# Performance work log

Measured on AMD Instinct MI355X. Metric: run time of the kernel, lower is better.

## Reference

```python
import jax, jax.numpy as jnp
import numpy as np

T, A, E, N, W, HID, FD = 4096, 1024, 512, 32768, 10, 150, 20
GI = 2 * A + E  # 2560
BINS = jnp.array([1, 2, 3, 4, 8, 16, 32, 64], dtype=jnp.int32)


def _mlp(x, W1, b1, W2, b2, W3, b3):
    # Score module: Linear->ReLU->Linear->ReLU->Linear->1 (dropout is a no-op in eval)
    h = jax.nn.relu(x @ W1 + b1)
    h = jax.nn.relu(h @ W2 + b2)
    return h @ W3 + b3


def setup_inputs() -> dict:
    key = jax.random.key(0)
    ks = jax.random.split(key, 20)
    s = 0.02
    inp = {
        "states": jax.random.normal(ks[0], (T, A), jnp.float32),
        "embeds": jax.random.normal(ks[1], (T, E), jnp.float32),
        "span_starts": jax.random.randint(ks[2], (N,), 0, T - W, jnp.int32),
        "span_widths": jax.random.randint(ks[3], (N,), 1, W + 1, jnp.int32),
        # attention Score params (input A)
        "Wa1": jax.random.normal(ks[4], (A, HID)) * s, "ba1": jnp.zeros((HID,)),
        "Wa2": jax.random.normal(ks[5], (HID, HID)) * s, "ba2": jnp.zeros((HID,)),
        "Wa3": jax.random.normal(ks[6], (HID, 1)) * s, "ba3": jnp.zeros((1,)),
        # width Feature embedding table: len(bins)+1 = 9 rows
        "width_emb": jax.random.normal(ks[7], (9, FD)) * s,
        # mention Score params (input GI + FD)
        "Ws1": jax.random.normal(ks[8], (GI + FD, HID)) * s, "bs1": jnp.zeros((HID,)),
        "Ws2": jax.random.normal(ks[9], (HID, HID)) * s, "bs2": jnp.zeros((HID,)),
        "Ws3": jax.random.normal(ks[10], (HID, 1)) * s, "bs3": jnp.zeros((1,)),
    }
    return inp


def reference(states, embeds, span_starts, span_widths,
              Wa1, ba1, Wa2, ba2, Wa3, ba3, width_emb,
              Ws1, bs1, Ws2, bs2, Ws3, bs3):
    # per-token attention logits  [T]
    attns = _mlp(states, Wa1, ba1, Wa2, ba2, Wa3, ba3).squeeze(-1)
    offs = jnp.arange(W)                                   # [W]
    pos = span_starts[:, None] + offs[None, :]             # [N, W]
    mask = offs[None, :] < span_widths[:, None]            # ragged span mask
    pos_c = jnp.clip(pos, 0, T - 1)
    logit = jnp.where(mask, attns[pos_c], -jnp.inf)        # [N, W]
    w = jax.nn.softmax(logit, axis=1)                      # per-span softmax
    attn_sum = jnp.einsum('nw,nwe->ne', w, embeds[pos_c])  # [N, E]
    ends = span_starts + span_widths - 1
    bin_idx = jnp.sum(span_widths[:, None] >= BINS[None, :], axis=1)
    size = width_emb[bin_idx]                              # [N, FD]
    g = jnp.concatenate([states[span_starts], states[ends], attn_sum, size], axis=1)
    scores = _mlp(g, Ws1, bs1, Ws2, bs2, Ws3, bs3).squeeze(-1)  # [N]
    return scores
```

## Files before the change

kernel.cpp:

```cpp
#include <hip/hip_runtime.h>
#include <math.h>

#define T_TOK 4096
#define A_DIM 1024
#define E_DIM 512
#define N_SPAN 32768
#define W_MAX 10
#define HID 150
#define FD 20

#define PR  160
#define KP2 160

#define WS_ATTNS 0
#define WS_PB    4096
#define WS_WPACK 1314816
#define WS_SB    1627856
#define WS_EB    3725008
#define PB_P0 0
#define PB_P1 655360
#define PB_P2 1310720
#define PB_P3 1966080
#define WP_ST  0
#define WP_V   491520
#define WP_A2  573440
#define WP_S2  599040
#define WP_WE1 624640
#define WP_TOTAL 626080
#define SB_PIECES 524288
#define EB_PIECES 262144
#define PK_ITEMS (WP_TOTAL + SB_PIECES + EB_PIECES)

typedef short  bf16x8 __attribute__((ext_vector_type(8)));
typedef float  f32x4  __attribute__((ext_vector_type(4)));

__device__ __forceinline__ float4 ld4(const float* p) { return *(const float4*)p; }

__device__ __forceinline__ unsigned short f2bf(float f) {
    unsigned u = __float_as_uint(f);
    unsigned r = u + 0x7fffu + ((u >> 16) & 1u);
    return (unsigned short)(r >> 16);
}
__device__ __forceinline__ float bf2f(short s) {
    return __uint_as_float(((unsigned)(unsigned short)s) << 16);
}
__device__ __forceinline__ bf16x8 cvt_frag(const float* p) {
    float4 u = ld4(p), v = ld4(p + 4);
    bf16x8 f;
    f[0] = (short)f2bf(u.x); f[1] = (short)f2bf(u.y);
    f[2] = (short)f2bf(u.z); f[3] = (short)f2bf(u.w);
    f[4] = (short)f2bf(v.x); f[5] = (short)f2bf(v.y);
    f[6] = (short)f2bf(v.z); f[7] = (short)f2bf(v.w);
    return f;
}

typedef const __attribute__((address_space(1))) unsigned int as1_u32;
typedef __attribute__((address_space(3))) unsigned int as3_u32;
__device__ __forceinline__ void dma16(const void* g, void* l) {
    __builtin_amdgcn_global_load_lds((as1_u32*)g, (as3_u32*)l, 16, 0, 0);
}
template<int N> __device__ __forceinline__ void waitv() {
    asm volatile("s_waitcnt vmcnt(%0)" :: "n"(N) : "memory");
}

__global__ __launch_bounds__(256) void prepack_kernel(
    const float* __restrict__ states, const float* __restrict__ embeds,
    const float* __restrict__ Wa1, const float* __restrict__ Ws1,
    const float* __restrict__ Wa2, const float* __restrict__ Ws2,
    const float* __restrict__ width_emb,
    unsigned short* __restrict__ wp, unsigned short* __restrict__ Sb,
    unsigned short* __restrict__ Eb)
{
    int idx = blockIdx.x * 256 + threadIdx.x;
    if (idx >= PK_ITEMS) return;
    if (idx < WP_TOTAL) {
        float v = 0.f;
        if (idx < WP_V) {
            int gidx = idx / 163840, r = idx % 163840;
            int ngrp = r / 81920, r2 = r % 81920;
            int c = r2 / 2560, d = r2 % 2560;
            int n = d >> 5, qsw = (d >> 3) & 3, off = d & 7;
            int q = qsw ^ ((n >> 1) & 3);
            int k = c * 32 + q * 8 + off;
            int gn = ngrp * 80 + n;
            const float* W = (gidx == 0) ? Wa1 : Ws1 + (size_t)(gidx - 1) * 1024 * HID;
            if (gn < HID) v = W[(size_t)k * HID + gn];
        } else if (idx < WP_A2) {
            int r = idx - WP_V;
            int ngrp = r / 40960, r2 = r % 40960;
            int c = r2 / 2560, d = r2 % 2560;
            int n = d >> 5, qsw = (d >> 3) & 3, off = d & 7;
            int q = qsw ^ ((n >> 1) & 3);
            int k = c * 32 + q * 8 + off;
            int gn = ngrp * 80 + n;
            if (gn < HID) v = Ws1[(size_t)(2048 + k) * HID + gn];
        } else if (idx < WP_S2) {
            int e = idx - WP_A2;
            int n = e / KP2, k = e % KP2;
            if (n < HID && k < HID) v = Wa2[(size_t)k * HID + n];
        } else if (idx < WP_WE1) {
            int e = idx - WP_S2;
            int n = e / KP2, k = e % KP2;
            if (n < HID && k < HID) v = Ws2[(size_t)k * HID + n];
        } else {
            int e = idx - WP_WE1;
            int b = e / KP2, n = e % KP2;
            if (n < HID)
                for (int k = 0; k < FD; ++k)
                    v = fmaf(width_emb[b * FD + k], Ws1[(size_t)(2560 + k) * HID + n], v);
        }
        wp[idx] = f2bf(v);
    } else if (idx < WP_TOTAL + SB_PIECES) {
        int p = idx - WP_TOTAL;
        int mb = p >> 11, r = p & 2047;
        int c = r >> 6, d8 = r & 63;
        int m = d8 >> 2, qsw = d8 & 3;
        int q = qsw ^ ((m >> 1) & 3);
        const float* src = states + (size_t)(mb * 16 + m) * A_DIM + c * 32 + q * 8;
        *(bf16x8*)(Sb + (size_t)p * 8) = cvt_frag(src);
    } else {
        int p = idx - WP_TOTAL - SB_PIECES;
        int mb = p >> 10, r = p & 1023;
        int c = r >> 6, d8 = r & 63;
        int m = d8 >> 2, qsw = d8 & 3;
        int q = qsw ^ ((m >> 1) & 3);
        const float* src = embeds + (size_t)(mb * 16 + m) * E_DIM + c * 32 + q * 8;
        *(bf16x8*)(Eb + (size_t)p * 8) = cvt_frag(src);
    }
}

template<int NC>
__device__ __forceinline__ void gemm_dma(
    const unsigned short* __restrict__ srcA, const unsigned short* __restrict__ srcB,
    unsigned short (*__restrict__ bufB)[2560], unsigned short (*__restrict__ bufA)[512],
    int lane, int l15, int quad, f32x4 (&acc)[5])
{
    const int swz = (quad ^ ((l15 >> 1) & 3)) * 8;
    const int bl = l15 * 32 + swz;
#define DMAC(c) { _Pragma("unroll")                                          \
        for (int i = 0; i < 5; ++i)                                          \
            dma16(srcB + (size_t)(c) * 2560 + i * 512 + lane * 8,            \
                  &bufB[(c) % 3][i * 512]);                                  \
        dma16(srcA + (size_t)(c) * 512 + lane * 8, &bufA[(c) % 3][0]); }
    DMAC(0);
    DMAC(1);
#pragma unroll
    for (int c = 0; c < NC; ++c) {
        if (c + 2 < NC) DMAC(c + 2);
        if (c + 2 < NC)      waitv<12>();
        else if (c + 1 < NC) waitv<6>();
        else                 waitv<0>();
        bf16x8 af = *(const bf16x8*)(&bufA[c % 3][0] + bl);
        const unsigned short* bb = &bufB[c % 3][0];
#pragma unroll
        for (int t = 0; t < 5; ++t) {
            bf16x8 bf = *(const bf16x8*)(bb + t * 512 + bl);
            acc[t] = __builtin_amdgcn_mfma_f32_16x16x32_bf16(af, bf, acc[t], 0, 0, 0);
        }
    }
#undef DMAC
}

__global__ __launch_bounds__(128) void token_kernel(
    const unsigned short* __restrict__ Sb, const unsigned short* __restrict__ Eb,
    const unsigned short* __restrict__ wp, unsigned short* __restrict__ Pb,
    const float* __restrict__ ba1, const float* __restrict__ ba2,
    const float* __restrict__ Wa3, const float* __restrict__ ba3,
    float* __restrict__ attns)
{
    __shared__ __align__(16) unsigned short bufB[2][3][2560];
    __shared__ __align__(16) unsigned short bufA[2][3][512];
    __shared__ float sPartA[2][16];

    const int wv = threadIdx.x >> 6;
    const int lane = threadIdx.x & 63, l15 = lane & 15, quad = lane >> 4;
    const int task = blockIdx.x;
    const int ngrp = wv;

    f32x4 acc[5];
#pragma unroll
    for (int t = 0; t < 5; ++t)
#pragma unroll
        for (int i = 0; i < 4; ++i) acc[t][i] = 0.f;

    int m0, gidx;
    if (task < 768) {
        const int mb = task / 3;
        m0 = mb * 16;
        gidx = task % 3;
        const unsigned short* srcA = Sb + (size_t)mb * 16384;
        const unsigned short* srcB = wp + WP_ST + gidx * 163840 + ngrp * 81920;
        gemm_dma<32>(srcA, srcB, bufB[wv], bufA[wv], lane, l15, quad, acc);
    } else {
        const int mb = task - 768;
        m0 = mb * 16;
        gidx = 3;
        const unsigned short* srcA = Eb + (size_t)mb * 8192;
        const unsigned short* srcB = wp + WP_V + ngrp * 40960;
        gemm_dma<16>(srcA, srcB, bufB[wv], bufA[wv], lane, l15, quad, acc);
    }

    if (gidx == 0) {
        unsigned short (*sHb)[168] = (unsigned short (*)[168])&bufB[0][0][0];
        __syncthreads();
#pragma unroll
        for (int t = 0; t < 5; ++t) {
            const int col = ngrp * 80 + t * 16 + l15;
            const float b1 = (col < HID) ? ba1[col] : 0.f;
#pragma unroll
            for (int i = 0; i < 4; ++i)
                sHb[quad * 4 + i][col] = f2bf(fmaxf(acc[t][i] + b1, 0.f));
        }
        __syncthreads();
        f32x4 a2[5];
#pragma unroll
        for (int t = 0; t < 5; ++t)
#pragma unroll
            for (int i = 0; i < 4; ++i) a2[t][i] = 0.f;
#pragma unroll
        for (int c = 0; c < 5; ++c) {
            const int kq = c * 32 + quad * 8;
            bf16x8 af = *(const bf16x8*)&sHb[l15][kq];
#pragma unroll
            for (int t = 0; t < 5; ++t) {
                const int nt = ngrp * 5 + t;
                bf16x8 bf = *(const bf16x8*)(wp + WP_A2 +
                            (size_t)(nt * 16 + l15) * KP2 + kq);
                a2[t] = __builtin_amdgcn_mfma_f32_16x16x32_bf16(af, bf, a2[t], 0, 0, 0);
            }
        }
        float sc[4] = {0.f, 0.f, 0.f, 0.f};
#pragma unroll
        for (int t = 0; t < 5; ++t) {
            const int col = (ngrp * 5 + t) * 16 + l15;
            const float w3 = (col < HID) ? Wa3[col] : 0.f;
            const float b2 = (col < HID) ? ba2[col] : 0.f;
#pragma unroll
            for (int i = 0; i < 4; ++i)
                sc[i] = fmaf(fmaxf(a2[t][i] + b2, 0.f), w3, sc[i]);
        }
#pragma unroll
        for (int off = 8; off >= 1; off >>= 1)
#pragma unroll
            for (int i = 0; i < 4; ++i) sc[i] += __shfl_down(sc[i], off, 16);
        if (l15 == 0)
#pragma unroll
            for (int i = 0; i < 4; ++i) sPartA[ngrp][quad * 4 + i] = sc[i];
        __syncthreads();
        if (threadIdx.x < 16)
            attns[m0 + threadIdx.x] =
                sPartA[0][threadIdx.x] + sPartA[1][threadIdx.x] + ba3[0];
    } else {
        unsigned short* Pg = Pb + (size_t)gidx * 655360;
#pragma unroll
        for (int t = 0; t < 5; ++t) {
            const int col = ngrp * 80 + t * 16 + l15;
#pragma unroll
            for (int i = 0; i < 4; ++i)
                Pg[(size_t)(m0 + quad * 4 + i) * PR + col] =
                    (col < HID) ? f2bf(acc[t][i]) : (unsigned short)0;
        }
    }
}

__global__ __launch_bounds__(256) void span_kernel(
    const unsigned short* __restrict__ Pb, const float* __restrict__ attns,
    const unsigned short* __restrict__ wp,
    const int* __restrict__ span_starts, const int* __restrict__ span_widths,
    const float* __restrict__ bs1, const float* __restrict__ bs2,
    const float* __restrict__ Ws3, const float* __restrict__ bs3,
    float* __restrict__ out)
{
    __shared__ unsigned short sHb[32][168];
    __shared__ float s_wgt[32][W_MAX];
    __shared__ int s_st[32], s_wd[32], s_bin[32], s_oid[32], s_wdr[32];
    __shared__ float sPart[4][32];
    __shared__ float sb1[KP2];

    const int tid = threadIdx.x;
    const int n0s = blockIdx.x * 32;

    if (tid < KP2) sb1[tid] = (tid < HID) ? bs1[tid] : 0.f;
    int st = 0, wd = 0;
    if (tid < 32) {
        st = span_starts[n0s + tid];
        wd = span_widths[n0s + tid];
        s_wdr[tid] = wd;
    }
    __syncthreads();
    if (tid < 32) {
        int rank = 0;
#pragma unroll
        for (int j = 0; j < 32; ++j) {
            const int wj = s_wdr[j];
            rank += (wj < wd) || (wj == wd && j < tid);
        }
        s_st[rank] = st; s_wd[rank] = wd; s_oid[rank] = tid;
        s_bin[rank] = (wd >= 1) + (wd >= 2) + (wd >= 3) + (wd >= 4) +
                      (wd >= 8) + (wd >= 16) + (wd >= 32) + (wd >= 64);
        float lg[W_MAX];
        float m = -1e30f;
#pragma unroll
        for (int w = 0; w < W_MAX; ++w)
            if (w < wd) { float a = attns[st + w]; lg[w] = a; m = fmaxf(m, a); }
        float sum = 0.f;
#pragma unroll
        for (int w = 0; w < W_MAX; ++w) {
            float e = (w < wd) ? __expf(lg[w] - m) : 0.f;
            lg[w] = e; sum += e;
        }
        float inv = 1.f / sum;
#pragma unroll
        for (int w = 0; w < W_MAX; ++w) s_wgt[rank][w] = lg[w] * inv;
    }
    __syncthreads();

    {
        const unsigned short* P1b = Pb + PB_P1;
        const unsigned short* P2b = Pb + PB_P2;
        const unsigned short* P3b = Pb + PB_P3;
        const unsigned short* WEb = wp + WP_WE1;
        const int s = tid >> 3, jl = tid & 7;
        const int sst = s_st[s], swd = s_wd[s];
        const size_t rs = (size_t)sst * PR;
        const size_t re = (size_t)(sst + swd - 1) * PR;
        const size_t rb = (size_t)s_bin[s] * PR;
        for (int c = jl; c < 20; c += 8) {
            const int j = c * 8;
            bf16x8 u1 = *(const bf16x8*)(P1b + rs + j);
            bf16x8 u2 = *(const bf16x8*)(P2b + re + j);
            bf16x8 uw = *(const bf16x8*)(WEb + rb + j);
            float acc[8];
#pragma unroll
            for (int i = 0; i < 8; ++i)
                acc[i] = bf2f(u1[i]) + bf2f(u2[i]) + bf2f(uw[i]) + sb1[j + i];
#pragma unroll
            for (int w = 0; w < W_MAX; ++w) {
                if (w < swd) {
                    float wt = s_wgt[s][w];
                    bf16x8 uv = *(const bf16x8*)(P3b + rs + (size_t)w * PR + j);
#pragma unroll
                    for (int i = 0; i < 8; ++i)
                        acc[i] = fmaf(wt, bf2f(uv[i]), acc[i]);
                }
            }
            bf16x8 pk;
#pragma unroll
            for (int i = 0; i < 8; ++i) pk[i] = (short)f2bf(fmaxf(acc[i], 0.f));
            *(bf16x8*)&sHb[s][j] = pk;
        }
    }
    __syncthreads();

    const int wv = tid >> 6, lane = tid & 63, l15 = lane & 15, quad = lane >> 4;
    const int nb = (wv < 2) ? wv * 3 : 6 + (wv - 2) * 2;
    const int cnt = (wv < 2) ? 3 : 2;

    f32x4 a2[2][3];
#pragma unroll
    for (int mt = 0; mt < 2; ++mt)
#pragma unroll
        for (int t = 0; t < 3; ++t)
#pragma unroll
            for (int i = 0; i < 4; ++i) a2[mt][t][i] = 0.f;

#pragma unroll
    for (int c = 0; c < 5; ++c) {
        int k0 = c * 32;
        bf16x8 af0 = *(const bf16x8*)&sHb[l15][k0 + quad * 8];
        bf16x8 af1 = *(const bf16x8*)&sHb[16 + l15][k0 + quad * 8];
#pragma unroll
        for (int t = 0; t < 3; ++t) {
            if (t < cnt) {
                bf16x8 b = *(const bf16x8*)(wp + WP_S2 +
                            (size_t)((nb + t) * 16 + l15) * KP2 + k0 + quad * 8);
                a2[0][t] = __builtin_amdgcn_mfma_f32_16x16x32_bf16(af0, b, a2[0][t], 0, 0, 0);
                a2[1][t] = __builtin_amdgcn_mfma_f32_16x16x32_bf16(af1, b, a2[1][t], 0, 0, 0);
            }
        }
    }

    float sc[2][4];
#pragma unroll
    for (int mt = 0; mt < 2; ++mt)
#pragma unroll
        for (int i = 0; i < 4; ++i) sc[mt][i] = 0.f;
#pragma unroll
    for (int t = 0; t < 3; ++t) {
        if (t < cnt) {
            int col = (nb + t) * 16 + l15;
            float w3 = (col < HID) ? Ws3[col] : 0.f;
            float b2 = (col < HID) ? bs2[col] : 0.f;
#pragma unroll
            for (int mt = 0; mt < 2; ++mt)
#pragma unroll
                for (int i = 0; i < 4; ++i)
                    sc[mt][i] = fmaf(fmaxf(a2[mt][t][i] + b2, 0.f), w3, sc[mt][i]);
        }
    }
#pragma unroll
    for (int off = 8; off >= 1; off >>= 1)
#pragma unroll
        for (int mt = 0; mt < 2; ++mt)
#pragma unroll
            for (int i = 0; i < 4; ++i)
                sc[mt][i] += __shfl_down(sc[mt][i], off, 16);
    if (l15 == 0) {
#pragma unroll
        for (int mt = 0; mt < 2; ++mt)
#pragma unroll
            for (int i = 0; i < 4; ++i)
                sPart[wv][mt * 16 + quad * 4 + i] = sc[mt][i];
    }
    __syncthreads();
    if (tid < 32)
        out[n0s + s_oid[tid]] = sPart[0][tid] + sPart[1][tid] + sPart[2][tid] +
                                sPart[3][tid] + bs3[0];
}

extern "C" void kernel_launch(void* const* d_in, const int* in_sizes, int n_in,
                              void* d_out, int out_size, void* d_ws, size_t ws_size,
                              hipStream_t stream)
{
    const float* states      = (const float*)d_in[0];
    const float* embeds      = (const float*)d_in[1];
    const int*   span_starts = (const int*)d_in[2];
    const int*   span_widths = (const int*)d_in[3];
    const float* Wa1 = (const float*)d_in[4];
    const float* ba1 = (const float*)d_in[5];
    const float* Wa2 = (const float*)d_in[6];
    const float* ba2 = (const float*)d_in[7];
    const float* Wa3 = (const float*)d_in[8];
    const float* ba3 = (const float*)d_in[9];
    const float* width_emb = (const float*)d_in[10];
    const float* Ws1 = (const float*)d_in[11];
    const float* bs1 = (const float*)d_in[12];
    const float* Ws2 = (const float*)d_in[13];
    const float* bs2 = (const float*)d_in[14];
    const float* Ws3 = (const float*)d_in[15];
    const float* bs3 = (const float*)d_in[16];
    float* out = (float*)d_out;

    float* ws    = (float*)d_ws;
    float* attns = ws + WS_ATTNS;
    unsigned short* Pb    = (unsigned short*)(ws + WS_PB);
    unsigned short* wpack = (unsigned short*)(ws + WS_WPACK);
    unsigned short* Sb    = (unsigned short*)(ws + WS_SB);
    unsigned short* Eb    = (unsigned short*)(ws + WS_EB);

    hipLaunchKernelGGL(prepack_kernel, dim3((PK_ITEMS + 255) / 256), dim3(256), 0, stream,
                       states, embeds, Wa1, Ws1, Wa2, Ws2, width_emb,
                       wpack, Sb, Eb);
    hipLaunchKernelGGL(token_kernel, dim3(1024), dim3(128), 0, stream,
                       Sb, Eb, wpack, Pb, ba1, ba2, Wa3, ba3, attns);
    hipLaunchKernelGGL(span_kernel, dim3(N_SPAN / 32), dim3(256), 0, stream,
                       Pb, attns, wpack, span_starts, span_widths,
                       bs1, bs2, Ws3, bs3, out);
}
```

Baseline: 139.9 us.

## Fuse fp32-to-bf16 activation conversion into token GEMM A-operand loads

Removes the prepack pass that converted states and embeds to swizzled bf16 buffers. The token GEMM now loads fp32 activations straight from global memory into registers, two float4 per chunk with a three-deep register prefetch, and converts them to bf16 before the MFMA. This drops a full read and write of the activations plus the A-side LDS staging. In exchange, each of the three column-group tasks that share a row block re-reads the fp32 rows, so global A traffic per task doubles, and register pressure rises.

```diff
diff --git a/kernel.cpp b/kernel.cpp
--- a/kernel.cpp
+++ b/kernel.cpp
@@ -15,8 +15,6 @@
 #define WS_ATTNS 0
 #define WS_PB    4096
 #define WS_WPACK 1314816
-#define WS_SB    1627856
-#define WS_EB    3725008
 #define PB_P0 0
 #define PB_P1 655360
 #define PB_P2 1310720
@@ -27,9 +25,6 @@
 #define WP_S2  599040
 #define WP_WE1 624640
 #define WP_TOTAL 626080
-#define SB_PIECES 524288
-#define EB_PIECES 262144
-#define PK_ITEMS (WP_TOTAL + SB_PIECES + EB_PIECES)
 
 typedef short  bf16x8 __attribute__((ext_vector_type(8)));
 typedef float  f32x4  __attribute__((ext_vector_type(4)));
@@ -44,15 +39,6 @@
 __device__ __forceinline__ float bf2f(short s) {
     return __uint_as_float(((unsigned)(unsigned short)s) << 16);
 }
-__device__ __forceinline__ bf16x8 cvt_frag(const float* p) {
-    float4 u = ld4(p), v = ld4(p + 4);
-    bf16x8 f;
-    f[0] = (short)f2bf(u.x); f[1] = (short)f2bf(u.y);
-    f[2] = (short)f2bf(u.z); f[3] = (short)f2bf(u.w);
-    f[4] = (short)f2bf(v.x); f[5] = (short)f2bf(v.y);
-    f[6] = (short)f2bf(v.z); f[7] = (short)f2bf(v.w);
-    return f;
-}
 
 typedef const __attribute__((address_space(1))) unsigned int as1_u32;
 typedef __attribute__((address_space(3))) unsigned int as3_u32;
@@ -64,93 +50,81 @@
 }
 
 __global__ __launch_bounds__(256) void prepack_kernel(
-    const float* __restrict__ states, const float* __restrict__ embeds,
     const float* __restrict__ Wa1, const float* __restrict__ Ws1,
     const float* __restrict__ Wa2, const float* __restrict__ Ws2,
     const float* __restrict__ width_emb,
-    unsigned short* __restrict__ wp, unsigned short* __restrict__ Sb,
-    unsigned short* __restrict__ Eb)
+    unsigned short* __restrict__ wp)
 {
     int idx = blockIdx.x * 256 + threadIdx.x;
-    if (idx >= PK_ITEMS) return;
-    if (idx < WP_TOTAL) {
-        float v = 0.f;
-        if (idx < WP_V) {
-            int gidx = idx / 163840, r = idx % 163840;
-            int ngrp = r / 81920, r2 = r % 81920;
-            int c = r2 / 2560, d = r2 % 2560;
-            int n = d >> 5, qsw = (d >> 3) & 3, off = d & 7;
-            int q = qsw ^ ((n >> 1) & 3);
-            int k = c * 32 + q * 8 + off;
-            int gn = ngrp * 80 + n;
-            const float* W = (gidx == 0) ? Wa1 : Ws1 + (size_t)(gidx - 1) * 1024 * HID;
-            if (gn < HID) v = W[(size_t)k * HID + gn];
-        } else if (idx < WP_A2) {
-            int r = idx - WP_V;
-            int ngrp = r / 40960, r2 = r % 40960;
-            int c = r2 / 2560, d = r2 % 2560;
-            int n = d >> 5, qsw = (d >> 3) & 3, off = d & 7;
-            int q = qsw ^ ((n >> 1) & 3);
-            int k = c * 32 + q * 8 + off;
-            int gn = ngrp * 80 + n;
-            if (gn < HID) v = Ws1[(size_t)(2048 + k) * HID + gn];
-        } else if (idx < WP_S2) {
-            int e = idx - WP_A2;
-            int n = e / KP2, k = e % KP2;
-            if (n < HID && k < HID) v = Wa2[(size_t)k * HID + n];
-        } else if (idx < WP_WE1) {
-            int e = idx - WP_S2;
-            int n = e / KP2, k = e % KP2;
-            if (n < HID && k < HID) v = Ws2[(size_t)k * HID + n];
-        } else {
-            int e = idx - WP_WE1;
-            int b = e / KP2, n = e % KP2;
-            if (n < HID)
-                for (int k = 0; k < FD; ++k)
-                    v = fmaf(width_emb[b * FD + k], Ws1[(size_t)(2560 + k) * HID + n], v);
-        }
-        wp[idx] = f2bf(v);
-    } else if (idx < WP_TOTAL + SB_PIECES) {
-        int p = idx - WP_TOTAL;
-        int mb = p >> 11, r = p & 2047;
-        int c = r >> 6, d8 = r & 63;
-        int m = d8 >> 2, qsw = d8 & 3;
-        int q = qsw ^ ((m >> 1) & 3);
-        const float* src = states + (size_t)(mb * 16 + m) * A_DIM + c * 32 + q * 8;
-        *(bf16x8*)(Sb + (size_t)p * 8) = cvt_frag(src);
+    if (idx >= WP_TOTAL) return;
+    float v = 0.f;
+    if (idx < WP_V) {
+        int gidx = idx / 163840, r = idx % 163840;
+        int ngrp = r / 81920, r2 = r % 81920;
+        int c = r2 / 2560, d = r2 % 2560;
+        int n = d >> 5, qsw = (d >> 3) & 3, off = d & 7;
+        int q = qsw ^ ((n >> 1) & 3);
+        int k = c * 32 + q * 8 + off;
+        int gn = ngrp * 80 + n;
+        const float* W = (gidx == 0) ? Wa1 : Ws1 + (size_t)(gidx - 1) * 1024 * HID;
+        if (gn < HID) v = W[(size_t)k * HID + gn];
+    } else if (idx < WP_A2) {
+        int r = idx - WP_V;
+        int ngrp = r / 40960, r2 = r % 40960;
+        int c = r2 / 2560, d = r2 % 2560;
+        int n = d >> 5, qsw = (d >> 3) & 3, off = d & 7;
+        int q = qsw ^ ((n >> 1) & 3);
+        int k = c * 32 + q * 8 + off;
+        int gn = ngrp * 80 + n;
+        if (gn < HID) v = Ws1[(size_t)(2048 + k) * HID + gn];
+    } else if (idx < WP_S2) {
+        int e = idx - WP_A2;
+        int n = e / KP2, k = e % KP2;
+        if (n < HID && k < HID) v = Wa2[(size_t)k * HID + n];
+    } else if (idx < WP_WE1) {
+        int e = idx - WP_S2;
+        int n = e / KP2, k = e % KP2;
+        if (n < HID && k < HID) v = Ws2[(size_t)k * HID + n];
     } else {
-        int p = idx - WP_TOTAL - SB_PIECES;
-        int mb = p >> 10, r = p & 1023;
-        int c = r >> 6, d8 = r & 63;
-        int m = d8 >> 2, qsw = d8 & 3;
-        int q = qsw ^ ((m >> 1) & 3);
-        const float* src = embeds + (size_t)(mb * 16 + m) * E_DIM + c * 32 + q * 8;
-        *(bf16x8*)(Eb + (size_t)p * 8) = cvt_frag(src);
-    }
-}
-
-template<int NC>
-__device__ __forceinline__ void gemm_dma(
-    const unsigned short* __restrict__ srcA, const unsigned short* __restrict__ srcB,
-    unsigned short (*__restrict__ bufB)[2560], unsigned short (*__restrict__ bufA)[512],
+        int e = idx - WP_WE1;
+        int b = e / KP2, n = e % KP2;
+        if (n < HID)
+            for (int k = 0; k < FD; ++k)
+                v = fmaf(width_emb[b * FD + k], Ws1[(size_t)(2560 + k) * HID + n], v);
+    }
+    wp[idx] = f2bf(v);
+}
+
+template<int NC, int LDA>
+__device__ __forceinline__ void gemm_direct(
+    const float* __restrict__ srcA, const unsigned short* __restrict__ srcB,
+    unsigned short (*__restrict__ bufB)[2560],
     int lane, int l15, int quad, f32x4 (&acc)[5])
 {
     const int swz = (quad ^ ((l15 >> 1) & 3)) * 8;
     const int bl = l15 * 32 + swz;
-#define DMAC(c) { _Pragma("unroll")                                          \
+    const float* aptr = srcA + (size_t)l15 * LDA + quad * 8;
+    float4 a0[3], a1[3];
+#define DMAB(c) { _Pragma("unroll")                                          \
         for (int i = 0; i < 5; ++i)                                          \
             dma16(srcB + (size_t)(c) * 2560 + i * 512 + lane * 8,            \
-                  &bufB[(c) % 3][i * 512]);                                  \
-        dma16(srcA + (size_t)(c) * 512 + lane * 8, &bufA[(c) % 3][0]); }
-    DMAC(0);
-    DMAC(1);
+                  &bufB[(c) % 3][i * 512]); }
+#define LDA_(c) { a0[(c) % 3] = ld4(aptr + (c) * 32);                        \
+                  a1[(c) % 3] = ld4(aptr + (c) * 32 + 4); }
+    DMAB(0); LDA_(0);
+    DMAB(1); LDA_(1);
 #pragma unroll
     for (int c = 0; c < NC; ++c) {
-        if (c + 2 < NC) DMAC(c + 2);
-        if (c + 2 < NC)      waitv<12>();
-        else if (c + 1 < NC) waitv<6>();
+        if (c + 2 < NC) { DMAB(c + 2); LDA_(c + 2); }
+        if (c + 2 < NC)      waitv<14>();
+        else if (c + 1 < NC) waitv<7>();
         else                 waitv<0>();
-        bf16x8 af = *(const bf16x8*)(&bufA[c % 3][0] + bl);
+        float4 u = a0[c % 3], v = a1[c % 3];
+        bf16x8 af;
+        af[0] = (short)f2bf(u.x); af[1] = (short)f2bf(u.y);
+        af[2] = (short)f2bf(u.z); af[3] = (short)f2bf(u.w);
+        af[4] = (short)f2bf(v.x); af[5] = (short)f2bf(v.y);
+        af[6] = (short)f2bf(v.z); af[7] = (short)f2bf(v.w);
         const unsigned short* bb = &bufB[c % 3][0];
 #pragma unroll
         for (int t = 0; t < 5; ++t) {
@@ -158,18 +132,18 @@
             acc[t] = __builtin_amdgcn_mfma_f32_16x16x32_bf16(af, bf, acc[t], 0, 0, 0);
         }
     }
-#undef DMAC
+#undef DMAB
+#undef LDA_
 }
 
 __global__ __launch_bounds__(128) void token_kernel(
-    const unsigned short* __restrict__ Sb, const unsigned short* __restrict__ Eb,
+    const float* __restrict__ states, const float* __restrict__ embeds,
     const unsigned short* __restrict__ wp, unsigned short* __restrict__ Pb,
     const float* __restrict__ ba1, const float* __restrict__ ba2,
     const float* __restrict__ Wa3, const float* __restrict__ ba3,
     float* __restrict__ attns)
 {
     __shared__ __align__(16) unsigned short bufB[2][3][2560];
-    __shared__ __align__(16) unsigned short bufA[2][3][512];
     __shared__ float sPartA[2][16];
 
     const int wv = threadIdx.x >> 6;
@@ -188,16 +162,16 @@
         const int mb = task / 3;
         m0 = mb * 16;
         gidx = task % 3;
-        const unsigned short* srcA = Sb + (size_t)mb * 16384;
+        const float* srcA = states + (size_t)mb * 16 * A_DIM;
         const unsigned short* srcB = wp + WP_ST + gidx * 163840 + ngrp * 81920;
-        gemm_dma<32>(srcA, srcB, bufB[wv], bufA[wv], lane, l15, quad, acc);
+        gemm_direct<32, A_DIM>(srcA, srcB, bufB[wv], lane, l15, quad, acc);
     } else {
         const int mb = task - 768;
         m0 = mb * 16;
         gidx = 3;
-        const unsigned short* srcA = Eb + (size_t)mb * 8192;
+        const float* srcA = embeds + (size_t)mb * 16 * E_DIM;
         const unsigned short* srcB = wp + WP_V + ngrp * 40960;
-        gemm_dma<16>(srcA, srcB, bufB[wv], bufA[wv], lane, l15, quad, acc);
+        gemm_direct<16, E_DIM>(srcA, srcB, bufB[wv], lane, l15, quad, acc);
     }
 
     if (gidx == 0) {
@@ -435,8 +409,8 @@
     const float* width_emb = (const float*)d_in[10];
     const float* Ws1 = (const float*)d_in[11];
     const float* bs1 = (const float*)d_in[12];
+    const float* bs2 = (const float*)d_in[14];
     const float* Ws2 = (const float*)d_in[13];
-    const float* bs2 = (const float*)d_in[14];
     const float* Ws3 = (const float*)d_in[15];
     const float* bs3 = (const float*)d_in[16];
     float* out = (float*)d_out;
@@ -445,14 +419,11 @@
     float* attns = ws + WS_ATTNS;
     unsigned short* Pb    = (unsigned short*)(ws + WS_PB);
     unsigned short* wpack = (unsigned short*)(ws + WS_WPACK);
-    unsigned short* Sb    = (unsigned short*)(ws + WS_SB);
-    unsigned short* Eb    = (unsigned short*)(ws + WS_EB);
-
-    hipLaunchKernelGGL(prepack_kernel, dim3((PK_ITEMS + 255) / 256), dim3(256), 0, stream,
-                       states, embeds, Wa1, Ws1, Wa2, Ws2, width_emb,
-                       wpack, Sb, Eb);
+
+    hipLaunchKernelGGL(prepack_kernel, dim3((WP_TOTAL + 255) / 256), dim3(256), 0, stream,
+                       Wa1, Ws1, Wa2, Ws2, width_emb, wpack);
     hipLaunchKernelGGL(token_kernel, dim3(1024), dim3(128), 0, stream,
-                       Sb, Eb, wpack, Pb, ba1, ba2, Wa3, ba3, attns);
+                       states, embeds, wpack, Pb, ba1, ba2, Wa3, ba3, attns);
     hipLaunchKernelGGL(span_kernel, dim3(N_SPAN / 32), dim3(256), 0, stream,
                        Pb, attns, wpack, span_starts, span_widths,
                        bs1, bs2, Ws3, bs3, out);
```

After: 145.4 us. 1.04x slower.
